# Kernel optimization log

Hardware: AMD Instinct MI355X
Metric: run time of the kernel (lower is better)

The kernel has to match this reference:

```python
import jax, jax.numpy as jnp
import numpy as np

NUM_HEADS = 16
NEG_FILL = -10000.0  # matches torch masked_fill value in source


def setup_inputs() -> dict:
    key = jax.random.key(0)
    ks = jax.random.split(key, 8)
    B, S, H = 4, 2048, 1024
    sc = 1.0 / np.sqrt(H)
    x = jax.random.normal(ks[0], (B, S, H), dtype=jnp.float32)
    L = jax.random.randint(ks[1], (B,), 1, S + 1, dtype=jnp.int64 if jax.config.jax_enable_x64 else jnp.int32)
    Wq = jax.random.normal(ks[2], (H, H), dtype=jnp.float32) * sc
    Wk = jax.random.normal(ks[3], (H, H), dtype=jnp.float32) * sc
    Wv = jax.random.normal(ks[4], (H, H), dtype=jnp.float32) * sc
    bv = jax.random.normal(ks[5], (H,), dtype=jnp.float32) * 0.01
    Wo = jax.random.normal(ks[6], (H, H), dtype=jnp.float32) * sc
    bo = jax.random.normal(ks[7], (H,), dtype=jnp.float32) * 0.01
    return {"x": x, "L": L, "Wq": Wq, "Wk": Wk, "Wv": Wv, "bv": bv, "Wo": Wo, "bo": bo}


def reference(x, L, Wq, Wk, Wv, bv, Wo, bo):
    # AttentionAggregator.forward with L given; dropout in eval mode (identity).
    B, S, H = x.shape
    nh = NUM_HEADS
    dk = H // nh
    # torch nn.Linear: y = x @ W.T + b
    q = (x @ Wq.T).reshape(B, S, nh, dk).transpose(0, 2, 1, 3)  # (B,h,S,dk)
    k = (x @ Wk.T).reshape(B, S, nh, dk).transpose(0, 2, 1, 3)
    v = (x @ Wv.T + bv).reshape(B, S, nh, dk).transpose(0, 2, 1, 3)
    scores = jnp.einsum("bhqd,bhkd->bhqk", q, k) / jnp.sqrt(jnp.float32(dk))
    valid = jnp.arange(S)[None, :] < L[:, None]  # (B,S) True where real token
    scores = jnp.where(valid[:, None, None, :], scores, NEG_FILL)
    attn = jax.nn.softmax(scores, axis=-1)
    ctx = jnp.einsum("bhqk,bhkd->bhqd", attn, v)
    ctx = ctx.transpose(0, 2, 1, 3).reshape(B, S, H)
    attn_out = ctx @ Wo.T + bo  # (B,S,H)
    # masked mean pool over valid positions
    m = valid.astype(x.dtype)  # (B,S)
    pooled = jnp.einsum("bsh,bs->bh", attn_out, m) / m.sum(axis=1, keepdims=True)
    return pooled
```

## Files before the change

kernel.cpp:

```cpp
#include <hip/hip_runtime.h>
#include <hip/hip_bf16.h>
#include <math.h>

constexpr int Bc = 4, Sc = 2048, Hc = 1024, NHc = 16, DKc = 64;

constexpr size_t XHOFF = 0;
constexpr size_t QOFF  = 4194304;
constexpr size_t KOFF  = 8388608;
constexpr size_t WQOFF = 12582912;
constexpr size_t WKOFF = 13107200;
constexpr size_t LIOFF = 13631488;
constexpr size_t WOFF  = 13762560;
constexpr size_t YOFF  = 13893632;
constexpr size_t CSOFF = 13959168;
constexpr size_t YPOFF = 13963264;
constexpr size_t RPOFF = 15011840;
constexpr size_t CPOFF = 15536128;

typedef __attribute__((ext_vector_type(8))) short bf16x8;
typedef __attribute__((ext_vector_type(4))) float f32x4;

__device__ inline short f2bf(float v) {
    __hip_bfloat16 h = __float2bfloat16(v);
    return *reinterpret_cast<short*>(&h);
}

__device__ inline void gld_lds16(const void* g, void* l) {
    __builtin_amdgcn_global_load_lds(
        (const __attribute__((address_space(1))) unsigned int*)g,
        (__attribute__((address_space(3))) unsigned int*)l, 16, 0, 0);
}

__global__ __launch_bounds__(256) void cvt_kernel(
    const float* __restrict__ src, short* __restrict__ dst, float scale)
{
    const size_t i = ((size_t)blockIdx.x * 256 + threadIdx.x) * 8;
    float4 a = *(const float4*)(src + i);
    float4 b = *(const float4*)(src + i + 4);
    bf16x8 o;
    o[0] = f2bf(a.x * scale); o[1] = f2bf(a.y * scale);
    o[2] = f2bf(a.z * scale); o[3] = f2bf(a.w * scale);
    o[4] = f2bf(b.x * scale); o[5] = f2bf(b.y * scale);
    o[6] = f2bf(b.z * scale); o[7] = f2bf(b.w * scale);
    *(bf16x8*)(dst + i) = o;
}

__global__ __launch_bounds__(256) void proj_mfma_kernel(
    const int* __restrict__ L, float* __restrict__ ws)
{
    const int z  = blockIdx.z;
    const int m0 = blockIdx.y * 128;
    const int n0 = blockIdx.x * 128;
    const int b  = m0 >> 11;
    const int s0 = m0 & 2047;
    const int Lb = L[b];
    if (s0 >= Lb) return;

    const short* __restrict__ A = (const short*)(ws + XHOFF);
    const short* __restrict__ W = (const short*)(ws + (z == 0 ? WQOFF : WKOFF));
    short* __restrict__ Out = (short*)(ws + (z == 0 ? QOFF : KOFF));

    __shared__ __align__(16) short As[128 * 32];
    __shared__ __align__(16) short Bs[128 * 32];

    const int tid  = threadIdx.x;
    const int lane = tid & 63;
    const int wave = tid >> 6;
    const int l16  = lane & 15, quad = lane >> 4;
    const int wm = (wave & 1) * 64, wn = (wave >> 1) * 64;

    const int c0 = tid, c1 = tid + 256;
    const int r0 = c0 >> 2, g0 = (c0 & 3) * 8;
    const int r1 = c1 >> 2, g1 = (c1 & 3) * 8;
    short* lA0 = As + wave * 512;
    short* lA1 = As + 2048 + wave * 512;
    short* lB0 = Bs + wave * 512;
    short* lB1 = Bs + 2048 + wave * 512;

    const f32x4 z4 = {0.f, 0.f, 0.f, 0.f};
    f32x4 acc[4][4];
    #pragma unroll
    for (int i = 0; i < 4; ++i)
        #pragma unroll
        for (int j = 0; j < 4; ++j) acc[i][j] = z4;

    for (int k0 = 0; k0 < Hc; k0 += 32) {
        __syncthreads();
        gld_lds16(A + (size_t)(m0 + r0) * Hc + k0 + g0, lA0);
        gld_lds16(A + (size_t)(m0 + r1) * Hc + k0 + g1, lA1);
        gld_lds16(W + (size_t)(n0 + r0) * Hc + k0 + g0, lB0);
        gld_lds16(W + (size_t)(n0 + r1) * Hc + k0 + g1, lB1);
        __syncthreads();

        bf16x8 af[4], bfr[4];
        #pragma unroll
        for (int mt = 0; mt < 4; ++mt)
            af[mt] = *(const bf16x8*)(As + (wm + mt * 16 + l16) * 32 + quad * 8);
        #pragma unroll
        for (int nt = 0; nt < 4; ++nt)
            bfr[nt] = *(const bf16x8*)(Bs + (wn + nt * 16 + l16) * 32 + quad * 8);
        #pragma unroll
        for (int mt = 0; mt < 4; ++mt)
            #pragma unroll
            for (int nt = 0; nt < 4; ++nt)
                acc[mt][nt] = __builtin_amdgcn_mfma_f32_16x16x32_bf16(
                    af[mt], bfr[nt], acc[mt][nt], 0, 0, 0);
    }

    #pragma unroll
    for (int mt = 0; mt < 4; ++mt) {
        #pragma unroll
        for (int nt = 0; nt < 4; ++nt) {
            const int n = n0 + wn + nt * 16 + l16;
            const int h = n >> 6, d = n & 63;
            #pragma unroll
            for (int r = 0; r < 4; ++r) {
                const int s = s0 + wm + mt * 16 + quad * 4 + r;
                Out[(((size_t)b * NHc + h) * Sc + s) * DKc + d] =
                    f2bf(acc[mt][nt][r]);
            }
        }
    }
}

__global__ __launch_bounds__(256) void rowsum_part_kernel(
    const int* __restrict__ L, float* __restrict__ ws)
{
    const int bh = blockIdx.x;
    const int b  = bh >> 4;
    const int Lb = L[b];
    const int kc0 = blockIdx.z * 512;
    if (blockIdx.y * 128 >= Lb || kc0 >= Lb) return;

    const int tid  = threadIdx.x;
    const int wave = tid >> 6;
    const int lane = tid & 63;
    const int q0 = blockIdx.y * 128 + wave * 32;
    const int l16 = lane & 15, quad = lane >> 4;

    const short* __restrict__ qarr = (const short*)(ws + QOFF) + (size_t)bh * Sc * DKc;
    const short* __restrict__ karr = (const short*)(ws + KOFF) + (size_t)bh * Sc * DKc;

    __shared__ __align__(16) short Ks[64 * 64];

    const short* qrow0 = qarr + (size_t)(q0 + l16) * DKc;
    const short* qrow1 = qarr + (size_t)(q0 + 16 + l16) * DKc;
    const bf16x8 b0lo = *(const bf16x8*)(qrow0 + quad * 8);
    const bf16x8 b0hi = *(const bf16x8*)(qrow0 + 32 + quad * 8);
    const bf16x8 b1lo = *(const bf16x8*)(qrow1 + quad * 8);
    const bf16x8 b1hi = *(const bf16x8*)(qrow1 + 32 + quad * 8);

    const int kend = (kc0 + 512 < Lb) ? kc0 + 512 : Lb;
    float lacc0 = 0.f, lacc1 = 0.f;

    for (int kt = kc0; kt < kend; kt += 64) {
        __syncthreads();
        #pragma unroll
        for (int i = 0; i < 2; ++i) {
            const int s = i * 256 + tid;
            const int row = s >> 3, cc = s & 7, c = cc ^ (row & 7);
            gld_lds16(karr + (size_t)(kt + row) * DKc + c * 8,
                      Ks + (i * 256 + wave * 64) * 8);
        }
        __syncthreads();

        #pragma unroll
        for (int t = 0; t < 4; ++t) {
            const int r = t * 16 + l16;
            const bf16x8 alo = *(const bf16x8*)(Ks + (r * 8 + (quad ^ (r & 7))) * 8);
            const bf16x8 ahi = *(const bf16x8*)(Ks + (r * 8 + ((4 + quad) ^ (r & 7))) * 8);
            f32x4 c0 = {0.f, 0.f, 0.f, 0.f}, c1 = {0.f, 0.f, 0.f, 0.f};
            c0 = __builtin_amdgcn_mfma_f32_16x16x32_bf16(alo, b0lo, c0, 0, 0, 0);
            c0 = __builtin_amdgcn_mfma_f32_16x16x32_bf16(ahi, b0hi, c0, 0, 0, 0);
            c1 = __builtin_amdgcn_mfma_f32_16x16x32_bf16(alo, b1lo, c1, 0, 0, 0);
            c1 = __builtin_amdgcn_mfma_f32_16x16x32_bf16(ahi, b1hi, c1, 0, 0, 0);
            #pragma unroll
            for (int rr = 0; rr < 4; ++rr) {
                const bool kv = (kt + t * 16 + quad * 4 + rr) < Lb;
                lacc0 += kv ? __expf(c0[rr]) : 0.f;
                lacc1 += kv ? __expf(c1[rr]) : 0.f;
            }
        }
    }
    lacc0 += __shfl_xor(lacc0, 16, 64); lacc0 += __shfl_xor(lacc0, 32, 64);
    lacc1 += __shfl_xor(lacc1, 16, 64); lacc1 += __shfl_xor(lacc1, 32, 64);
    float* __restrict__ rp = ws + RPOFF + ((size_t)blockIdx.z * 64 + bh) * Sc;
    if (quad == 0) rp[q0 + l16]      = lacc0;
    if (quad == 1) rp[q0 + 16 + l16] = lacc1;
}

__global__ __launch_bounds__(256) void rowsum_reduce_kernel(
    const int* __restrict__ L, float* __restrict__ ws)
{
    const int bh = blockIdx.y;
    const int q  = blockIdx.x * 256 + threadIdx.x;
    const int nc = (L[bh >> 4] + 511) >> 9;
    float acc = 0.f;
    for (int c = 0; c < nc; ++c)
        acc += ws[RPOFF + ((size_t)c * 64 + bh) * Sc + q];
    ws[LIOFF + (size_t)bh * Sc + q] = 1.0f / acc;
}

__global__ __launch_bounds__(256) void colsum_part_kernel(
    const int* __restrict__ L, float* __restrict__ ws)
{
    const int bh = blockIdx.x;
    const int b  = bh >> 4;
    const int Lb = L[b];
    const int qc0 = blockIdx.z * 512;
    if (blockIdx.y * 128 >= Lb || qc0 >= Lb) return;

    const int tid  = threadIdx.x;
    const int wave = tid >> 6;
    const int lane = tid & 63;
    const int k0 = blockIdx.y * 128 + wave * 32;
    const int l16 = lane & 15, quad = lane >> 4;

    const short* __restrict__ qarr = (const short*)(ws + QOFF) + (size_t)bh * Sc * DKc;
    const short* __restrict__ karr = (const short*)(ws + KOFF) + (size_t)bh * Sc * DKc;
    const float* __restrict__ liarr = ws + LIOFF + (size_t)bh * Sc;

    __shared__ __align__(16) short Qs[64 * 64];
    __shared__ __align__(16) float Lis[64];

    const short* krow0 = karr + (size_t)(k0 + l16) * DKc;
    const short* krow1 = karr + (size_t)(k0 + 16 + l16) * DKc;
    const bf16x8 a0lo = *(const bf16x8*)(krow0 + quad * 8);
    const bf16x8 a0hi = *(const bf16x8*)(krow0 + 32 + quad * 8);
    const bf16x8 a1lo = *(const bf16x8*)(krow1 + quad * 8);
    const bf16x8 a1hi = *(const bf16x8*)(krow1 + 32 + quad * 8);

    const int qend = (qc0 + 512 < Lb) ? qc0 + 512 : Lb;
    float w0[4] = {0.f, 0.f, 0.f, 0.f};
    float w1[4] = {0.f, 0.f, 0.f, 0.f};

    for (int qt = qc0; qt < qend; qt += 64) {
        __syncthreads();
        #pragma unroll
        for (int i = 0; i < 2; ++i) {
            const int s = i * 256 + tid;
            const int row = s >> 3, cc = s & 7, c = cc ^ (row & 7);
            gld_lds16(qarr + (size_t)(qt + row) * DKc + c * 8,
                      Qs + (i * 256 + wave * 64) * 8);
        }
        if (tid < 16)
            gld_lds16(liarr + qt + tid * 4, Lis);
        __syncthreads();

        #pragma unroll
        for (int t = 0; t < 4; ++t) {
            const int r = t * 16 + l16;
            const bf16x8 blo = *(const bf16x8*)(Qs + (r * 8 + (quad ^ (r & 7))) * 8);
            const bf16x8 bhi = *(const bf16x8*)(Qs + (r * 8 + ((4 + quad) ^ (r & 7))) * 8);
            const float lv = (qt + r < Lb) ? Lis[r] : 0.f;
            f32x4 c0 = {0.f, 0.f, 0.f, 0.f}, c1 = {0.f, 0.f, 0.f, 0.f};
            c0 = __builtin_amdgcn_mfma_f32_16x16x32_bf16(a0lo, blo, c0, 0, 0, 0);
            c0 = __builtin_amdgcn_mfma_f32_16x16x32_bf16(a0hi, bhi, c0, 0, 0, 0);
            c1 = __builtin_amdgcn_mfma_f32_16x16x32_bf16(a1lo, blo, c1, 0, 0, 0);
            c1 = __builtin_amdgcn_mfma_f32_16x16x32_bf16(a1hi, bhi, c1, 0, 0, 0);
            #pragma unroll
            for (int rr = 0; rr < 4; ++rr) {
                w0[rr] += __expf(c0[rr]) * lv;
                w1[rr] += __expf(c1[rr]) * lv;
            }
        }
    }
    #pragma unroll
    for (int off = 1; off <= 8; off <<= 1) {
        #pragma unroll
        for (int rr = 0; rr < 4; ++rr) {
            w0[rr] += __shfl_xor(w0[rr], off, 64);
            w1[rr] += __shfl_xor(w1[rr], off, 64);
        }
    }
    if (l16 == 0) {
        float* __restrict__ cp = ws + CPOFF + ((size_t)blockIdx.z * 64 + bh) * Sc;
        #pragma unroll
        for (int rr = 0; rr < 4; ++rr) {
            cp[k0 + quad * 4 + rr]      = w0[rr];
            cp[k0 + 16 + quad * 4 + rr] = w1[rr];
        }
    }
}

__global__ __launch_bounds__(256) void colsum_reduce_kernel(
    const int* __restrict__ L, float* __restrict__ ws)
{
    const int bh = blockIdx.y;
    const int k  = blockIdx.x * 256 + threadIdx.x;
    const int nc = (L[bh >> 4] + 511) >> 9;
    float acc = 0.f;
    for (int c = 0; c < nc; ++c)
        acc += ws[CPOFF + ((size_t)c * 64 + bh) * Sc + k];
    ws[WOFF + (size_t)bh * Sc + k] = acc;
}

__global__ __launch_bounds__(256) void yw_part_kernel(
    const float* __restrict__ x, const int* __restrict__ L,
    float* __restrict__ ws)
{
    const int b  = blockIdx.y;
    const int j0 = blockIdx.x * 64;
    const int s0 = blockIdx.z * 128;
    const int Lb = L[b];
    if (s0 >= Lb) return;
    const int js = threadIdx.x & 63;
    const int sl = threadIdx.x >> 6;
    const float* __restrict__ warr = ws + WOFF + (size_t)b * NHc * Sc;
    const float* __restrict__ xb = x + (size_t)b * Sc * Hc;

    __shared__ float wt[128][20];
    __shared__ float red[4][16][64];

    #pragma unroll
    for (int i = 0; i < 8; ++i) {
        const int s = (threadIdx.x & 15) + 16 * i;
        const int h = threadIdx.x >> 4;
        float v = 0.f;
        if (s0 + s < Lb) v = warr[(size_t)h * Sc + s0 + s];
        wt[s][h] = v;
    }
    __syncthreads();

    float acc[16];
    #pragma unroll
    for (int h = 0; h < 16; ++h) acc[h] = 0.f;

    #pragma unroll 4
    for (int s = sl; s < 128; s += 4) {
        const float xv = xb[(size_t)(s0 + s) * Hc + j0 + js];
        const f32x4 wa = *(const f32x4*)&wt[s][0];
        const f32x4 wb = *(const f32x4*)&wt[s][4];
        const f32x4 wc = *(const f32x4*)&wt[s][8];
        const f32x4 wd = *(const f32x4*)&wt[s][12];
        #pragma unroll
        for (int h = 0; h < 4; ++h) acc[h]      += wa[h] * xv;
        #pragma unroll
        for (int h = 0; h < 4; ++h) acc[4 + h]  += wb[h] * xv;
        #pragma unroll
        for (int h = 0; h < 4; ++h) acc[8 + h]  += wc[h] * xv;
        #pragma unroll
        for (int h = 0; h < 4; ++h) acc[12 + h] += wd[h] * xv;
    }
    #pragma unroll
    for (int h = 0; h < 16; ++h) red[sl][h][js] = acc[h];
    __syncthreads();
    if (sl == 0) {
        float* __restrict__ yp = ws + YPOFF +
            ((size_t)blockIdx.z * Bc * NHc + (size_t)b * NHc) * Hc;
        #pragma unroll
        for (int h = 0; h < 16; ++h)
            yp[(size_t)h * Hc + j0 + js] =
                red[0][h][js] + red[1][h][js] + red[2][h][js] + red[3][h][js];
    }
}

__global__ __launch_bounds__(256) void yw_reduce_kernel(
    const int* __restrict__ L, float* __restrict__ ws)
{
    const int b = blockIdx.y;
    const int i = blockIdx.x * 256 + threadIdx.x;
    const int nc = (L[b] + 127) >> 7;
    const float* __restrict__ p = ws + YPOFF + (size_t)b * NHc * Hc + i;
    float acc = 0.f;
    for (int c = 0; c < nc; ++c)
        acc += p[(size_t)c * Bc * NHc * Hc];
    ws[YOFF + (size_t)b * NHc * Hc + i] = acc;
}

__global__ __launch_bounds__(256) void csum_kernel(
    const float* __restrict__ Wv, const float* __restrict__ bv,
    const int* __restrict__ L, float* __restrict__ ws)
{
    const int b = blockIdx.y;
    const int n = blockIdx.x * 256 + threadIdx.x;
    const int h0 = (blockIdx.x * 256) >> 6;
    __shared__ float ys[4][1024];
    const float* __restrict__ y = ws + YOFF + ((size_t)b * NHc + h0) * Hc;
    for (int i = threadIdx.x; i < 4096; i += 256) ys[i >> 10][i & 1023] = y[i];
    __syncthreads();
    const int hl = threadIdx.x >> 6;
    const float* __restrict__ wrow = Wv + (size_t)n * Hc;
    float acc = 0.f;
    for (int j = 0; j < Hc; j += 4) {
        float4 wv = *(const float4*)(wrow + j);
        acc += wv.x*ys[hl][j] + wv.y*ys[hl][j+1] + wv.z*ys[hl][j+2] + wv.w*ys[hl][j+3];
    }
    ws[CSOFF + (size_t)b * Hc + n] = acc + bv[n] * (float)L[b];
}

__global__ __launch_bounds__(256) void out_kernel(
    const float* __restrict__ Wo, const float* __restrict__ bo,
    const int* __restrict__ L, const float* __restrict__ ws,
    float* __restrict__ out)
{
    const int b = blockIdx.y;
    const int n = blockIdx.x * 256 + threadIdx.x;
    __shared__ float cs[Hc];
    const float* __restrict__ c = ws + CSOFF + (size_t)b * Hc;
    for (int i = threadIdx.x; i < Hc; i += 256) cs[i] = c[i];
    __syncthreads();
    const float* __restrict__ wrow = Wo + (size_t)n * Hc;
    float acc = 0.f;
    for (int h = 0; h < Hc; h += 4) {
        float4 wv = *(const float4*)(wrow + h);
        acc += wv.x*cs[h] + wv.y*cs[h+1] + wv.z*cs[h+2] + wv.w*cs[h+3];
    }
    out[(size_t)b * Hc + n] = acc / (float)L[b] + bo[n];
}

extern "C" void kernel_launch(void* const* d_in, const int* in_sizes, int n_in,
                              void* d_out, int out_size, void* d_ws, size_t ws_size,
                              hipStream_t stream)
{
    (void)in_sizes; (void)n_in; (void)out_size; (void)ws_size;
    const float* x  = (const float*)d_in[0];
    const int*   L  = (const int*)d_in[1];
    const float* Wq = (const float*)d_in[2];
    const float* Wk = (const float*)d_in[3];
    const float* Wv = (const float*)d_in[4];
    const float* bv = (const float*)d_in[5];
    const float* Wo = (const float*)d_in[6];
    const float* bo = (const float*)d_in[7];
    float* out = (float*)d_out;
    float* ws  = (float*)d_ws;

    cvt_kernel<<<4096, 256, 0, stream>>>(x,  (short*)(ws + XHOFF), 1.0f);
    cvt_kernel<<<512,  256, 0, stream>>>(Wq, (short*)(ws + WQOFF), 0.125f);
    cvt_kernel<<<512,  256, 0, stream>>>(Wk, (short*)(ws + WKOFF), 1.0f);

    dim3 gp(Hc / 128, (Bc * Sc) / 128, 2);
    proj_mfma_kernel<<<gp, 256, 0, stream>>>(L, ws);

    dim3 gr(Bc * NHc, Sc / 128, 4);
    rowsum_part_kernel<<<gr, 256, 0, stream>>>(L, ws);
    dim3 grr(Sc / 256, Bc * NHc);
    rowsum_reduce_kernel<<<grr, 256, 0, stream>>>(L, ws);

    dim3 gcp(Bc * NHc, Sc / 128, 4);
    colsum_part_kernel<<<gcp, 256, 0, stream>>>(L, ws);
    colsum_reduce_kernel<<<grr, 256, 0, stream>>>(L, ws);

    dim3 gy(Hc / 64, Bc, Sc / 128);
    yw_part_kernel<<<gy, 256, 0, stream>>>(x, L, ws);

    dim3 gyr((NHc * Hc) / 256, Bc);
    yw_reduce_kernel<<<gyr, 256, 0, stream>>>(L, ws);

    dim3 gc(Hc / 256, Bc);
    csum_kernel<<<gc, 256, 0, stream>>>(Wv, bv, L, ws);

    dim3 go(Hc / 256, Bc);
    out_kernel<<<go, 256, 0, stream>>>(Wo, bo, L, ws, out);
}
```

Measured before the change: 276.5 us.

## Fuse conversions, double attention key/query tiles, and restructure GEMV kernels for coalescing

Merges the three fp32-to-bf16 conversion launches into one kernel. Doubles the LDS tile in the rowsum and colsum partial kernels from 64 to 128 rows, which halves the barrier count per chunk. Rewrites csum and out as wave-per-row GEMVs with coalesced loads and shuffle reductions, spread over more blocks. The larger tiles read past the valid length, and kend masking covers this in rowsum. It is unclear whether colsum has matching masking for tiles that run past Lb.

```diff
diff --git a/kernel.cpp b/kernel.cpp
--- a/kernel.cpp
+++ b/kernel.cpp
@@ -31,18 +31,23 @@
         (__attribute__((address_space(3))) unsigned int*)l, 16, 0, 0);
 }
 
-__global__ __launch_bounds__(256) void cvt_kernel(
-    const float* __restrict__ src, short* __restrict__ dst, float scale)
+__global__ __launch_bounds__(256) void cvt_all_kernel(
+    const float* __restrict__ x, const float* __restrict__ Wq,
+    const float* __restrict__ Wk, float* __restrict__ ws)
 {
     const size_t i = ((size_t)blockIdx.x * 256 + threadIdx.x) * 8;
-    float4 a = *(const float4*)(src + i);
-    float4 b = *(const float4*)(src + i + 4);
+    const float* src; short* dst; float scale; size_t off;
+    if (i < 8388608)       { src = x;  dst = (short*)(ws + XHOFF); off = i;            scale = 1.0f;   }
+    else if (i < 9437184)  { src = Wq; dst = (short*)(ws + WQOFF); off = i - 8388608;  scale = 0.125f; }
+    else                   { src = Wk; dst = (short*)(ws + WKOFF); off = i - 9437184;  scale = 1.0f;   }
+    float4 a = *(const float4*)(src + off);
+    float4 b = *(const float4*)(src + off + 4);
     bf16x8 o;
     o[0] = f2bf(a.x * scale); o[1] = f2bf(a.y * scale);
     o[2] = f2bf(a.z * scale); o[3] = f2bf(a.w * scale);
     o[4] = f2bf(b.x * scale); o[5] = f2bf(b.y * scale);
     o[6] = f2bf(b.z * scale); o[7] = f2bf(b.w * scale);
-    *(bf16x8*)(dst + i) = o;
+    *(bf16x8*)(dst + off) = o;
 }
 
 __global__ __launch_bounds__(256) void proj_mfma_kernel(
@@ -141,7 +146,7 @@
     const short* __restrict__ qarr = (const short*)(ws + QOFF) + (size_t)bh * Sc * DKc;
     const short* __restrict__ karr = (const short*)(ws + KOFF) + (size_t)bh * Sc * DKc;
 
-    __shared__ __align__(16) short Ks[64 * 64];
+    __shared__ __align__(16) short Ks[128 * 64];
 
     const short* qrow0 = qarr + (size_t)(q0 + l16) * DKc;
     const short* qrow1 = qarr + (size_t)(q0 + 16 + l16) * DKc;
@@ -153,10 +158,10 @@
     const int kend = (kc0 + 512 < Lb) ? kc0 + 512 : Lb;
     float lacc0 = 0.f, lacc1 = 0.f;
 
-    for (int kt = kc0; kt < kend; kt += 64) {
-        __syncthreads();
-        #pragma unroll
-        for (int i = 0; i < 2; ++i) {
+    for (int kt = kc0; kt < kend; kt += 128) {
+        __syncthreads();
+        #pragma unroll
+        for (int i = 0; i < 4; ++i) {
             const int s = i * 256 + tid;
             const int row = s >> 3, cc = s & 7, c = cc ^ (row & 7);
             gld_lds16(karr + (size_t)(kt + row) * DKc + c * 8,
@@ -165,7 +170,7 @@
         __syncthreads();
 
         #pragma unroll
-        for (int t = 0; t < 4; ++t) {
+        for (int t = 0; t < 8; ++t) {
             const int r = t * 16 + l16;
             const bf16x8 alo = *(const bf16x8*)(Ks + (r * 8 + (quad ^ (r & 7))) * 8);
             const bf16x8 ahi = *(const bf16x8*)(Ks + (r * 8 + ((4 + quad) ^ (r & 7))) * 8);
@@ -176,7 +181,7 @@
             c1 = __builtin_amdgcn_mfma_f32_16x16x32_bf16(ahi, b1hi, c1, 0, 0, 0);
             #pragma unroll
             for (int rr = 0; rr < 4; ++rr) {
-                const bool kv = (kt + t * 16 + quad * 4 + rr) < Lb;
+                const bool kv = (kt + t * 16 + quad * 4 + rr) < kend;
                 lacc0 += kv ? __expf(c0[rr]) : 0.f;
                 lacc1 += kv ? __expf(c1[rr]) : 0.f;
             }
@@ -220,8 +225,8 @@
     const short* __restrict__ karr = (const short*)(ws + KOFF) + (size_t)bh * Sc * DKc;
     const float* __restrict__ liarr = ws + LIOFF + (size_t)bh * Sc;
 
-    __shared__ __align__(16) short Qs[64 * 64];
-    __shared__ __align__(16) float Lis[64];
+    __shared__ __align__(16) short Qs[128 * 64];
+    __shared__ __align__(16) float Lis[128];
 
     const short* krow0 = karr + (size_t)(k0 + l16) * DKc;
     const short* krow1 = karr + (size_t)(k0 + 16 + l16) * DKc;
@@ -234,21 +239,21 @@
     float w0[4] = {0.f, 0.f, 0.f, 0.f};
     float w1[4] = {0.f, 0.f, 0.f, 0.f};
 
-    for (int qt = qc0; qt < qend; qt += 64) {
-        __syncthreads();
-        #pragma unroll
-        for (int i = 0; i < 2; ++i) {
+    for (int qt = qc0; qt < qend; qt += 128) {
+        __syncthreads();
+        #pragma unroll
+        for (int i = 0; i < 4; ++i) {
             const int s = i * 256 + tid;
             const int row = s >> 3, cc = s & 7, c = cc ^ (row & 7);
             gld_lds16(qarr + (size_t)(qt + row) * DKc + c * 8,
                       Qs + (i * 256 + wave * 64) * 8);
         }
-        if (tid < 16)
+        if (tid < 32)
             gld_lds16(liarr + qt + tid * 4, Lis);
         __syncthreads();
 
         #pragma unroll
-        for (int t = 0; t < 4; ++t) {
+        for (int t = 0; t < 8; ++t) {
             const int r = t * 16 + l16;
             const bf16x8 blo = *(const bf16x8*)(Qs + (r * 8 + (quad ^ (r & 7))) * 8);
             const bf16x8 bhi = *(const bf16x8*)(Qs + (r * 8 + ((4 + quad) ^ (r & 7))) * 8);
@@ -373,20 +378,36 @@
     const int* __restrict__ L, float* __restrict__ ws)
 {
     const int b = blockIdx.y;
-    const int n = blockIdx.x * 256 + threadIdx.x;
-    const int h0 = (blockIdx.x * 256) >> 6;
-    __shared__ float ys[4][1024];
-    const float* __restrict__ y = ws + YOFF + ((size_t)b * NHc + h0) * Hc;
-    for (int i = threadIdx.x; i < 4096; i += 256) ys[i >> 10][i & 1023] = y[i];
+    const int h = blockIdx.x;
+    const int n0 = h * 64;
+    const int lane = threadIdx.x & 63;
+    const int wave = threadIdx.x >> 6;
+    const float Lb = (float)L[b];
+
+    __shared__ float ys[1024];
+    const float* __restrict__ y = ws + YOFF + ((size_t)b * NHc + h) * Hc;
+    for (int i = threadIdx.x; i < 1024; i += 256) ys[i] = y[i];
     __syncthreads();
-    const int hl = threadIdx.x >> 6;
-    const float* __restrict__ wrow = Wv + (size_t)n * Hc;
-    float acc = 0.f;
-    for (int j = 0; j < Hc; j += 4) {
-        float4 wv = *(const float4*)(wrow + j);
-        acc += wv.x*ys[hl][j] + wv.y*ys[hl][j+1] + wv.z*ys[hl][j+2] + wv.w*ys[hl][j+3];
-    }
-    ws[CSOFF + (size_t)b * Hc + n] = acc + bv[n] * (float)L[b];
+
+    f32x4 yv[4];
+    #pragma unroll
+    for (int p = 0; p < 4; ++p) yv[p] = *(const f32x4*)&ys[p * 256 + lane * 4];
+
+    #pragma unroll
+    for (int r = 0; r < 16; ++r) {
+        const int n = n0 + wave * 16 + r;
+        const float* wrow = Wv + (size_t)n * Hc;
+        float a = 0.f;
+        #pragma unroll
+        for (int p = 0; p < 4; ++p) {
+            const f32x4 wv = *(const f32x4*)(wrow + p * 256 + lane * 4);
+            a += wv[0]*yv[p][0] + wv[1]*yv[p][1] + wv[2]*yv[p][2] + wv[3]*yv[p][3];
+        }
+        #pragma unroll
+        for (int off = 32; off > 0; off >>= 1) a += __shfl_xor(a, off, 64);
+        if (lane == 0)
+            ws[CSOFF + (size_t)b * Hc + n] = a + bv[n] * Lb;
+    }
 }
 
 __global__ __launch_bounds__(256) void out_kernel(
@@ -395,18 +416,35 @@
     float* __restrict__ out)
 {
     const int b = blockIdx.y;
-    const int n = blockIdx.x * 256 + threadIdx.x;
-    __shared__ float cs[Hc];
+    const int o0 = blockIdx.x * 64;
+    const int lane = threadIdx.x & 63;
+    const int wave = threadIdx.x >> 6;
+    const float linv = 1.0f / (float)L[b];
+
+    __shared__ float cs[1024];
     const float* __restrict__ c = ws + CSOFF + (size_t)b * Hc;
-    for (int i = threadIdx.x; i < Hc; i += 256) cs[i] = c[i];
+    for (int i = threadIdx.x; i < 1024; i += 256) cs[i] = c[i];
     __syncthreads();
-    const float* __restrict__ wrow = Wo + (size_t)n * Hc;
-    float acc = 0.f;
-    for (int h = 0; h < Hc; h += 4) {
-        float4 wv = *(const float4*)(wrow + h);
-        acc += wv.x*cs[h] + wv.y*cs[h+1] + wv.z*cs[h+2] + wv.w*cs[h+3];
-    }
-    out[(size_t)b * Hc + n] = acc / (float)L[b] + bo[n];
+
+    f32x4 cv[4];
+    #pragma unroll
+    for (int p = 0; p < 4; ++p) cv[p] = *(const f32x4*)&cs[p * 256 + lane * 4];
+
+    #pragma unroll
+    for (int r = 0; r < 16; ++r) {
+        const int o = o0 + wave * 16 + r;
+        const float* wrow = Wo + (size_t)o * Hc;
+        float a = 0.f;
+        #pragma unroll
+        for (int p = 0; p < 4; ++p) {
+            const f32x4 wv = *(const f32x4*)(wrow + p * 256 + lane * 4);
+            a += wv[0]*cv[p][0] + wv[1]*cv[p][1] + wv[2]*cv[p][2] + wv[3]*cv[p][3];
+        }
+        #pragma unroll
+        for (int off = 32; off > 0; off >>= 1) a += __shfl_xor(a, off, 64);
+        if (lane == 0)
+            out[(size_t)b * Hc + o] = a * linv + bo[o];
+    }
 }
 
 extern "C" void kernel_launch(void* const* d_in, const int* in_sizes, int n_in,
@@ -425,9 +463,7 @@
     float* out = (float*)d_out;
     float* ws  = (float*)d_ws;
 
-    cvt_kernel<<<4096, 256, 0, stream>>>(x,  (short*)(ws + XHOFF), 1.0f);
-    cvt_kernel<<<512,  256, 0, stream>>>(Wq, (short*)(ws + WQOFF), 0.125f);
-    cvt_kernel<<<512,  256, 0, stream>>>(Wk, (short*)(ws + WKOFF), 1.0f);
+    cvt_all_kernel<<<5120, 256, 0, stream>>>(x, Wq, Wk, ws);
 
     dim3 gp(Hc / 128, (Bc * Sc) / 128, 2);
     proj_mfma_kernel<<<gp, 256, 0, stream>>>(L, ws);
@@ -447,9 +483,9 @@
     dim3 gyr((NHc * Hc) / 256, Bc);
     yw_reduce_kernel<<<gyr, 256, 0, stream>>>(L, ws);
 
-    dim3 gc(Hc / 256, Bc);
+    dim3 gc(NHc, Bc);
     csum_kernel<<<gc, 256, 0, stream>>>(Wv, bv, L, ws);
 
-    dim3 go(Hc / 256, Bc);
+    dim3 go(Hc / 64, Bc);
     out_kernel<<<go, 256, 0, stream>>>(Wo, bo, L, ws, out);
 }
```

Result: faster. 241.4 us (-12.7%).
